# Performance work log

Hardware: AMD Instinct MI355X
Metric: run time of the kernel (lower is better)

## Reference

```python
import jax, jax.numpy as jnp
import numpy as np

B, S, D, H = 4, 2048, 1024, 16
HD = D // H  # head_dim = 64

def setup_inputs() -> dict:
    key = jax.random.key(0)
    ks = jax.random.split(key, 6)
    scale = 1.0 / np.sqrt(D)
    x = jax.random.normal(ks[0], (B, S, D), dtype=jnp.float32)
    Wq = jax.random.normal(ks[1], (D, D), dtype=jnp.float32) * scale
    Wk = jax.random.normal(ks[2], (D, D), dtype=jnp.float32) * scale
    Wv = jax.random.normal(ks[3], (D, D), dtype=jnp.float32) * scale
    Wo = jax.random.normal(ks[4], (D, D), dtype=jnp.float32) * scale
    z = jnp.zeros((D,), dtype=jnp.float32)
    return {"x": x, "Wq": Wq, "bq": z, "Wk": Wk, "bk": z, "Wv": Wv, "bv": z, "Wo": Wo, "bo": z}

def reference(x, Wq, bq, Wk, bk, Wv, bv, Wo, bo):
    b, s, d = x.shape
    hd = d // H
    def split_heads(t):
        return t.reshape(b, s, H, hd).swapaxes(1, 2)  # [B,H,S,hd]
    q = split_heads(x @ Wq + bq)
    k = split_heads(x @ Wk + bk)
    v = split_heads(x @ Wv + bv)
    logits = jnp.einsum('bhqd,bhkd->bhqk', q, k) / jnp.sqrt(jnp.asarray(hd, x.dtype))
    attn = jax.nn.softmax(logits, axis=-1)
    vals = jnp.einsum('bhqk,bhkd->bhqd', attn, v)
    vals = vals.swapaxes(1, 2).reshape(b, s, d)
    return vals @ Wo + bo
```

## Files before the change

### kernel.cpp

```cpp
#include <hip/hip_runtime.h>
#include <hip/hip_bf16.h>
#include <cstdint>
#include <cstddef>


typedef __attribute__((ext_vector_type(8))) short short8;
typedef __attribute__((ext_vector_type(8))) unsigned short ushort8;
typedef __attribute__((ext_vector_type(4))) unsigned short ushort4v;
typedef __attribute__((ext_vector_type(4))) float floatx4;

#define LOG2E 1.44269504088896340736f
#define QSCALE (0.125f * LOG2E)

__device__ __forceinline__ unsigned short f2bf(float f) {
  union { float f; unsigned int u; } c; c.f = f;
  return (unsigned short)((c.u + 0x7fffu + ((c.u >> 16) & 1u)) >> 16);
}

__device__ __forceinline__ unsigned int pack_bf16(float a, float b) {
  unsigned int ua = __builtin_bit_cast(unsigned int, a) + 0x8000u;
  unsigned int ub = __builtin_bit_cast(unsigned int, b) + 0x8000u;
  return __builtin_amdgcn_perm(ub, ua, 0x07060302);
}

__device__ __forceinline__ float fexp2(float x) {
#if __HIP_DEVICE_COMPILE__
  return __builtin_amdgcn_exp2f(x);
#else
  return x;
#endif
}

__device__ __forceinline__ void gl_lds16(const void* g, void* l) {
  __builtin_amdgcn_global_load_lds((__attribute__((address_space(1))) void*)g,
                                   (__attribute__((address_space(3))) void*)l, 16, 0, 0);
}

__global__ __launch_bounds__(256) void cast_x_kernel(const float* __restrict__ x,
                                                     unsigned short* __restrict__ xb, int n4) {
  int i = blockIdx.x * 256 + threadIdx.x;
  if (i >= n4) return;
  float4 v = ((const float4*)x)[i];
  ushort4v o;
  o.x = f2bf(v.x); o.y = f2bf(v.y); o.z = f2bf(v.z); o.w = f2bf(v.w);
  ((ushort4v*)xb)[i] = o;
}

__global__ __launch_bounds__(256) void transpose_w_kernel(
    const float* __restrict__ Wq, const float* __restrict__ Wk,
    const float* __restrict__ Wv, const float* __restrict__ Wo,
    unsigned short* __restrict__ Wqkv_t, unsigned short* __restrict__ Wo_t) {
  __shared__ float tile[32][33];
  const int which = blockIdx.z;
  const float* src = (which == 0) ? Wq : (which == 1) ? Wk : (which == 2) ? Wv : Wo;
  unsigned short* dst = (which == 3) ? Wo_t : (Wqkv_t + (size_t)which * 1024 * 1024);
  const int bn = blockIdx.x * 32;
  const int bk = blockIdx.y * 32;
  const int tx = threadIdx.x & 31, ty = threadIdx.x >> 5;
#pragma unroll
  for (int r = 0; r < 32; r += 8)
    tile[ty + r][tx] = src[(size_t)(bk + ty + r) * 1024 + bn + tx];
  __syncthreads();
#pragma unroll
  for (int r = 0; r < 32; r += 8)
    dst[(size_t)(bn + ty + r) * 1024 + bk + tx] = f2bf(tile[tx][ty + r]);
}

template <int MODE>
__global__ __launch_bounds__(256, 3) void gemm_bt(
    const unsigned short* __restrict__ A, const unsigned short* __restrict__ Bt,
    int M, int N, int K,
    const float* __restrict__ bias0, const float* __restrict__ bias1,
    const float* __restrict__ bias2,
    unsigned short* __restrict__ outQ, unsigned short* __restrict__ outK,
    unsigned short* __restrict__ outVt, float* __restrict__ outF) {
  __shared__ unsigned short As[128 * 32];
  __shared__ unsigned short Bs[128 * 32];

  const int tid = threadIdx.x;
  const int lane = tid & 63;
  const int wid = tid >> 6;
  const int wm = wid >> 1, wn = wid & 1;
  const int l15 = lane & 15, q4 = lane >> 4;
  const int bm = blockIdx.x * 128, bn = blockIdx.y * 128;

  const int rowL = lane >> 2;
  const int segL = (lane & 3) * 16;

  const char* Ab = (const char*)A;
  const char* Bb = (const char*)Bt;
  const size_t strideA = (size_t)K * 2;

  floatx4 acc[4][4] = {};

  for (int k0 = 0; k0 < K; k0 += 32) {
    __syncthreads();
#pragma unroll
    for (int c0 = 0; c0 < 2; ++c0) {
      const int c = wid * 2 + c0;
      gl_lds16(Ab + (size_t)(bm + c * 16 + rowL) * strideA + (size_t)k0 * 2 + segL,
               &As[c * 512]);
      gl_lds16(Bb + (size_t)(bn + c * 16 + rowL) * strideA + (size_t)k0 * 2 + segL,
               &Bs[c * 512]);
    }
    __syncthreads();

    short8 af[4], bfr[4];
#pragma unroll
    for (int i = 0; i < 4; ++i)
      af[i] = *(const short8*)&As[(wm * 64 + i * 16 + l15) * 32 + q4 * 8];
#pragma unroll
    for (int j = 0; j < 4; ++j)
      bfr[j] = *(const short8*)&Bs[(wn * 64 + j * 16 + l15) * 32 + q4 * 8];
#pragma unroll
    for (int i = 0; i < 4; ++i)
#pragma unroll
      for (int j = 0; j < 4; ++j)
        acc[i][j] = __builtin_amdgcn_mfma_f32_16x16x32_bf16(af[i], bfr[j], acc[i][j], 0, 0, 0);
  }

  if (MODE == 0) {
    __syncthreads();
    unsigned short* scr = ((wid < 2) ? As : Bs) + (wid & 1) * 2048;
    const int region = bn >> 10;
    const float* bias = (region == 0) ? bias0 : (region == 1) ? bias1 : bias2;
    const int row0b = bm + wm * 64;
    const int b = row0b >> 11;
    const int colbase = (bn + wn * 64) & 1023;
    const int h = colbase >> 6;
    const size_t bh = (size_t)(b * 16 + h);
#pragma unroll
    for (int i = 0; i < 4; ++i) {
      const int s0 = (row0b + i * 16) & 2047;
#pragma unroll
      for (int j = 0; j < 4; ++j) {
        const int col = j * 16 + l15;
        const float bb = bias[colbase + col];
#pragma unroll
        for (int r = 0; r < 4; ++r) {
          float v = acc[i][j][r] + bb;
          if (region == 0) v *= QSCALE;
          scr[(q4 * 4 + r) * 66 + col] = f2bf(v);
        }
      }
      if (region <= 1) {
        unsigned short* dst = (region == 0) ? outQ : outK;
        ushort8 v0 = *(ushort8*)&scr[l15 * 66 + q4 * 16];
        ushort8 v1 = *(ushort8*)&scr[l15 * 66 + q4 * 16 + 8];
        unsigned short* orow = dst + (bh * 2048 + s0 + l15) * 64 + q4 * 16;
        *(ushort8*)orow = v0;
        *(ushort8*)(orow + 8) = v1;
      } else {
        const int hd = lane;
        unsigned short tmp[16];
#pragma unroll
        for (int r = 0; r < 16; ++r) tmp[r] = scr[r * 66 + hd];
        ushort8 v0, v1;
#pragma unroll
        for (int r = 0; r < 8; ++r) { v0[r] = tmp[r]; v1[r] = tmp[8 + r]; }
        unsigned short* orow = outVt + (bh * 64 + hd) * 2048 + s0;
        *(ushort8*)orow = v0;
        *(ushort8*)(orow + 8) = v1;
      }
      __syncthreads();
    }
  } else {
#pragma unroll
    for (int i = 0; i < 4; ++i) {
      const int row0 = bm + wm * 64 + i * 16 + q4 * 4;
#pragma unroll
      for (int j = 0; j < 4; ++j) {
        const int gn = bn + wn * 64 + j * 16 + l15;
        const float bb = bias0[gn];
#pragma unroll
        for (int r = 0; r < 4; ++r)
          outF[(size_t)(row0 + r) * N + gn] = acc[i][j][r] + bb;
      }
    }
  }
}

__global__ __launch_bounds__(256, 4) void flash_attn(
    const unsigned short* __restrict__ Q, const unsigned short* __restrict__ Kg,
    const unsigned short* __restrict__ Vt, unsigned short* __restrict__ Oout) {
  __shared__ __align__(128) unsigned short Ks[2][64 * 64];
  __shared__ __align__(128) unsigned short Vs[2][64 * 64];

  const int tid = threadIdx.x, lane = tid & 63, wid = tid >> 6;
  const int l15 = lane & 15, q4 = lane >> 4;

  const int lid = blockIdx.x;
  const int slot = lid >> 3;
  const int bh = (lid & 7) * 8 + (slot >> 4);
  const int q0 = (slot & 15) * 128;
  const int bb = bh >> 4, hh = bh & 15;
  const size_t base = (size_t)bh * 2048 * 64;

  short8 qf[2][2];
#pragma unroll
  for (int s = 0; s < 2; ++s) {
    const unsigned short* qrow = Q + base + (size_t)(q0 + s * 64 + wid * 16 + l15) * 64;
    qf[s][0] = *(const short8*)(qrow + q4 * 8);
    qf[s][1] = *(const short8*)(qrow + 32 + q4 * 8);
  }

  union { unsigned int u[4]; short8 v; } ov;
  ov.u[0] = 0x3F803F80u; ov.u[1] = 0x3F803F80u; ov.u[2] = 0x3F803F80u; ov.u[3] = 0x3F803F80u;
  const short8 onesf = ov.v;

  const int r0 = wid * 16 + (lane >> 3);
  const int sg2 = ((lane & 7) ^ ((lane >> 3) & 7)) * 8;
  auto gpf = [](int r) {
    const int loc = r & 31;
    return (r & 32) + ((loc >> 2) & 3) * 8 + ((loc >> 4) & 1) * 4 + (loc & 3);
  };
  const unsigned short* kc0 = Kg + base + (size_t)gpf(r0) * 64 + sg2;
  const unsigned short* kc1 = Kg + base + (size_t)gpf(r0 + 8) * 64 + sg2;
  const unsigned short* vc0 = Vt + base + (size_t)r0 * 2048 + sg2;
  const unsigned short* vc1 = vc0 + 8 * 2048;

  const int wofs = wid * 1024;
  auto stage = [&](int b) {
    gl_lds16(kc0, &Ks[b][wofs]);        gl_lds16(kc1, &Ks[b][wofs + 512]);
    gl_lds16(vc0, &Vs[b][wofs]);        gl_lds16(vc1, &Vs[b][wofs + 512]);
    kc0 += 4096; kc1 += 4096; vc0 += 64; vc1 += 64;
  };

  stage(0);

  floatx4 oacc[2][4] = {};
  floatx4 lacc[2] = {};
  const int fo0 = (q4 ^ (l15 & 7)) << 3;

  const int thr = l15 * 64;
  const unsigned short* kA = &Ks[0][thr + fo0];
  const unsigned short* kB = &Ks[0][thr + (fo0 ^ 32)];
  const unsigned short* vA = &Vs[0][thr + fo0];
  const unsigned short* vB = &Vs[0][thr + (fo0 ^ 32)];

  auto body = [&](int BUF) {
    short8 pf[2][2];
#pragma unroll
    for (int c = 0; c < 2; ++c) {
      floatx4 sc[2][2] = {};
#pragma unroll
      for (int tt = 0; tt < 2; ++tt) {
        const int t = 2 * c + tt;
        short8 kf0 = *(const short8*)(kA + BUF + t * 1024);
        short8 kf1 = *(const short8*)(kB + BUF + t * 1024);
        __builtin_amdgcn_s_setprio(1);
#pragma unroll
        for (int s = 0; s < 2; ++s) {
          sc[s][tt] = __builtin_amdgcn_mfma_f32_16x16x32_bf16(kf0, qf[s][0], sc[s][tt], 0, 0, 0);
          sc[s][tt] = __builtin_amdgcn_mfma_f32_16x16x32_bf16(kf1, qf[s][1], sc[s][tt], 0, 0, 0);
        }
        __builtin_amdgcn_s_setprio(0);
      }
#pragma unroll
      for (int s = 0; s < 2; ++s) {
        float e0 = fexp2(sc[s][0][0]), e1 = fexp2(sc[s][0][1]);
        float e2 = fexp2(sc[s][0][2]), e3 = fexp2(sc[s][0][3]);
        float e4 = fexp2(sc[s][1][0]), e5 = fexp2(sc[s][1][1]);
        float e6 = fexp2(sc[s][1][2]), e7 = fexp2(sc[s][1][3]);
        union { unsigned int u[4]; short8 v; } cv;
        cv.u[0] = pack_bf16(e0, e1); cv.u[1] = pack_bf16(e2, e3);
        cv.u[2] = pack_bf16(e4, e5); cv.u[3] = pack_bf16(e6, e7);
        pf[s][c] = cv.v;
        lacc[s] = __builtin_amdgcn_mfma_f32_16x16x32_bf16(onesf, pf[s][c], lacc[s], 0, 0, 0);
      }
    }

#pragma unroll
    for (int t = 0; t < 4; ++t) {
      short8 vf0 = *(const short8*)(vA + BUF + t * 1024);
      short8 vf1 = *(const short8*)(vB + BUF + t * 1024);
      __builtin_amdgcn_s_setprio(1);
#pragma unroll
      for (int s = 0; s < 2; ++s) {
        oacc[s][t] = __builtin_amdgcn_mfma_f32_16x16x32_bf16(vf0, pf[s][0], oacc[s][t], 0, 0, 0);
        oacc[s][t] = __builtin_amdgcn_mfma_f32_16x16x32_bf16(vf1, pf[s][1], oacc[s][t], 0, 0, 0);
      }
      __builtin_amdgcn_s_setprio(0);
    }
  };

  for (int ip = 0; ip < 16; ++ip) {
    __syncthreads();
    stage(1);
    body(0);
    __syncthreads();
    if (ip < 15) stage(0);
    body(4096);
  }

#pragma unroll
  for (int s = 0; s < 2; ++s) {
    const float inv = 1.0f / lacc[s][0];
    const int srow = q0 + s * 64 + wid * 16 + l15;
    unsigned short* orow = Oout + ((size_t)bb * 2048 + srow) * 1024 + hh * 64;
#pragma unroll
    for (int t = 0; t < 4; ++t) {
      union { unsigned int u[2]; ushort4v s4; } cv;
      cv.u[0] = pack_bf16(oacc[s][t][0] * inv, oacc[s][t][1] * inv);
      cv.u[1] = pack_bf16(oacc[s][t][2] * inv, oacc[s][t][3] * inv);
      *(ushort4v*)(orow + t * 16 + q4 * 4) = cv.s4;
    }
  }
}

extern "C" void kernel_launch(void* const* d_in, const int* in_sizes, int n_in,
                              void* d_out, int out_size, void* d_ws, size_t ws_size,
                              hipStream_t stream) {
  const float* x  = (const float*)d_in[0];
  const float* Wq = (const float*)d_in[1];
  const float* bq = (const float*)d_in[2];
  const float* Wk = (const float*)d_in[3];
  const float* bk = (const float*)d_in[4];
  const float* Wv = (const float*)d_in[5];
  const float* bv = (const float*)d_in[6];
  const float* Wo = (const float*)d_in[7];
  const float* bo = (const float*)d_in[8];
  float* out = (float*)d_out;

  char* ws = (char*)d_ws;
  unsigned short* xb     = (unsigned short*)(ws);
  unsigned short* wqkv_t = (unsigned short*)(ws + (16u << 20));
  unsigned short* wo_t   = (unsigned short*)(ws + (22u << 20));
  unsigned short* Qb     = (unsigned short*)(ws + (24u << 20));
  unsigned short* Kb     = (unsigned short*)(ws + (40u << 20));
  unsigned short* Vtb    = (unsigned short*)(ws + (56u << 20));
  unsigned short* attn   = (unsigned short*)(ws + (72u << 20));
  (void)in_sizes; (void)n_in; (void)out_size; (void)ws_size;

  cast_x_kernel<<<dim3(8192), 256, 0, stream>>>(x, xb, 8192 * 1024 / 4);
  transpose_w_kernel<<<dim3(32, 32, 4), 256, 0, stream>>>(Wq, Wk, Wv, Wo, wqkv_t, wo_t);
  gemm_bt<0><<<dim3(64, 24), 256, 0, stream>>>(xb, wqkv_t, 8192, 3072, 1024,
                                               bq, bk, bv, Qb, Kb, Vtb, nullptr);
  flash_attn<<<dim3(1024), 256, 0, stream>>>(Qb, Kb, Vtb, attn);
  gemm_bt<1><<<dim3(64, 8), 256, 0, stream>>>(attn, wo_t, 8192, 1024, 1024,
                                              bo, nullptr, nullptr,
                                              nullptr, nullptr, nullptr, out);
}
```

Before: 271.0 us.

## Replace QKV projection GEMM with 256x256-tile 8-wave pipelined kernel

Adds a dedicated QKV GEMM kernel that uses 512 threads and 256x256 output tiles with a 64-wide K step. It double-buffers A and B through XOR-swizzled LDS via direct global-to-LDS loads, interleaving staging with MFMA bursts under raised wave priority. Larger tiles raise operand reuse and cut global traffic, and the swizzle avoids LDS bank conflicts. The cost is heavy register and LDS use (128 KB shared), which limits occupancy, and only 384 blocks are launched.

```diff
diff --git a/kernel.cpp b/kernel.cpp
--- a/kernel.cpp
+++ b/kernel.cpp
@@ -66,14 +66,146 @@
     dst[(size_t)(bn + ty + r) * 1024 + bk + tx] = f2bf(tile[tx][ty + r]);
 }
 
+#define QKV_FIRE(B0, B1, J0)                                                            \
+  __builtin_amdgcn_s_barrier();                                                         \
+  asm volatile("s_waitcnt lgkmcnt(0)" ::: "memory");                                    \
+  __builtin_amdgcn_sched_barrier(0);                                                    \
+  __builtin_amdgcn_s_setprio(1);                                                        \
+  _Pragma("unroll")                                                                     \
+  for (int i_ = 0; i_ < 8; ++i_) {                                                      \
+    acc[i_][J0] = __builtin_amdgcn_mfma_f32_16x16x32_bf16(af[i_], B0, acc[i_][J0], 0, 0, 0); \
+    acc[i_][J0 + 1] =                                                                   \
+        __builtin_amdgcn_mfma_f32_16x16x32_bf16(af[i_], B1, acc[i_][J0 + 1], 0, 0, 0);  \
+  }                                                                                     \
+  __builtin_amdgcn_s_setprio(0);
+
+__global__ __launch_bounds__(512, 2) void gemm_qkv8(
+    const unsigned short* __restrict__ A, const unsigned short* __restrict__ Bt,
+    const float* __restrict__ bq, const float* __restrict__ bk, const float* __restrict__ bv,
+    unsigned short* __restrict__ outQ, unsigned short* __restrict__ outK,
+    unsigned short* __restrict__ outVt) {
+  __shared__ __align__(128) unsigned short S[65536];
+
+  const int tid = threadIdx.x, lane = tid & 63, wid = tid >> 6;
+  const int wm = wid >> 2, wn = wid & 3;
+  const int l15 = lane & 15, q4 = lane >> 4;
+  const int bm = blockIdx.x * 256, bn = blockIdx.y * 256;
+
+  const int srow = wid * 16 + (lane >> 3);
+  const int sgu = ((lane & 7) ^ ((lane >> 3) & 7)) * 8;
+  const unsigned short* pa00 = A + (size_t)(bm + srow) * 1024 + sgu;
+  const unsigned short* pa01 = pa00 + 8 * 1024;
+  const unsigned short* pa10 = pa00 + 128 * 1024;
+  const unsigned short* pa11 = pa00 + 136 * 1024;
+  const unsigned short* pb00 = Bt + (size_t)(bn + srow) * 1024 + sgu;
+  const unsigned short* pb01 = pb00 + 8 * 1024;
+  const unsigned short* pb10 = pb00 + 128 * 1024;
+  const unsigned short* pb11 = pb00 + 136 * 1024;
+
+  const int wdst = wid * 1024;
+  auto stageA = [&](const int SO) {
+    gl_lds16(pa00, &S[SO + wdst]);          gl_lds16(pa01, &S[SO + wdst + 512]);
+    gl_lds16(pa10, &S[SO + 8192 + wdst]);   gl_lds16(pa11, &S[SO + 8192 + wdst + 512]);
+    pa00 += 64; pa01 += 64; pa10 += 64; pa11 += 64;
+  };
+  auto stageB = [&](const int SO) {
+    gl_lds16(pb00, &S[32768 + SO + wdst]);        gl_lds16(pb01, &S[32768 + SO + wdst + 512]);
+    gl_lds16(pb10, &S[32768 + SO + 8192 + wdst]); gl_lds16(pb11, &S[32768 + SO + 8192 + wdst + 512]);
+    pb00 += 64; pb01 += 64; pb10 += 64; pb11 += 64;
+  };
+
+  const int fo0 = (q4 ^ (l15 & 7)) * 8;
+  const unsigned short* aP0 = S + wm * 8192 + l15 * 64 + fo0;
+  const unsigned short* aP1 = S + wm * 8192 + l15 * 64 + (fo0 ^ 32);
+  const unsigned short* bP0 = S + 32768 + (wn >> 1) * 8192 + ((wn & 1) * 64 + l15) * 64 + fo0;
+  const unsigned short* bP1 = S + 32768 + (wn >> 1) * 8192 + ((wn & 1) * 64 + l15) * 64 + (fo0 ^ 32);
+
+  floatx4 acc[8][4] = {};
+  short8 af[8];
+
+  stageA(0); stageB(0);
+  __syncthreads();
+
+  auto body = [&](const int RO, const int SO) {
+#pragma unroll
+    for (int i = 0; i < 8; ++i) af[i] = *(const short8*)(aP0 + RO + i * 1024);
+    short8 b0 = *(const short8*)(bP0 + RO);
+    short8 b1 = *(const short8*)(bP0 + RO + 1024);
+    stageA(SO);
+    QKV_FIRE(b0, b1, 0)
+    __builtin_amdgcn_s_barrier();
+    b0 = *(const short8*)(bP0 + RO + 2048);
+    b1 = *(const short8*)(bP0 + RO + 3072);
+    stageB(SO);
+    QKV_FIRE(b0, b1, 2)
+    __builtin_amdgcn_s_barrier();
+#pragma unroll
+    for (int i = 0; i < 8; ++i) af[i] = *(const short8*)(aP1 + RO + i * 1024);
+    b0 = *(const short8*)(bP1 + RO);
+    b1 = *(const short8*)(bP1 + RO + 1024);
+    QKV_FIRE(b0, b1, 0)
+    __builtin_amdgcn_s_barrier();
+    b0 = *(const short8*)(bP1 + RO + 2048);
+    b1 = *(const short8*)(bP1 + RO + 3072);
+    QKV_FIRE(b0, b1, 2)
+    __syncthreads();
+  };
+
+  for (int p = 0; p < 8; ++p) {
+    body(0, 16384);
+    body(16384, 0);
+  }
+
+  __syncthreads();
+  unsigned short* scr = S + wid * 1088;
+  const int region = bn >> 10;
+  const float* bias = (region == 0) ? bq : (region == 1) ? bk : bv;
+  const int row0b = bm + wm * 128;
+  const int b = row0b >> 11;
+  const int colbase = (bn + wn * 64) & 1023;
+  const int h = colbase >> 6;
+  const size_t bh = (size_t)(b * 16 + h);
+#pragma unroll
+  for (int i = 0; i < 8; ++i) {
+    const int s0 = (row0b + i * 16) & 2047;
+#pragma unroll
+    for (int j = 0; j < 4; ++j) {
+      const int col = j * 16 + l15;
+      const float bb = bias[colbase + col];
+#pragma unroll
+      for (int r = 0; r < 4; ++r) {
+        float v = acc[i][j][r] + bb;
+        if (region == 0) v *= QSCALE;
+        scr[(q4 * 4 + r) * 66 + col] = f2bf(v);
+      }
+    }
+    if (region <= 1) {
+      unsigned short* dst = (region == 0) ? outQ : outK;
+      ushort8 v0 = *(ushort8*)&scr[l15 * 66 + q4 * 16];
+      ushort8 v1 = *(ushort8*)&scr[l15 * 66 + q4 * 16 + 8];
+      unsigned short* orow = dst + (bh * 2048 + s0 + l15) * 64 + q4 * 16;
+      *(ushort8*)orow = v0;
+      *(ushort8*)(orow + 8) = v1;
+    } else {
+      const int hd = lane;
+      unsigned short tmp[16];
+#pragma unroll
+      for (int r = 0; r < 16; ++r) tmp[r] = scr[r * 66 + hd];
+      ushort8 v0, v1;
+#pragma unroll
+      for (int r = 0; r < 8; ++r) { v0[r] = tmp[r]; v1[r] = tmp[8 + r]; }
+      unsigned short* orow = outVt + (bh * 64 + hd) * 2048 + s0;
+      *(ushort8*)orow = v0;
+      *(ushort8*)(orow + 8) = v1;
+    }
+  }
+}
+
 template <int MODE>
 __global__ __launch_bounds__(256, 3) void gemm_bt(
     const unsigned short* __restrict__ A, const unsigned short* __restrict__ Bt,
     int M, int N, int K,
-    const float* __restrict__ bias0, const float* __restrict__ bias1,
-    const float* __restrict__ bias2,
-    unsigned short* __restrict__ outQ, unsigned short* __restrict__ outK,
-    unsigned short* __restrict__ outVt, float* __restrict__ outF) {
+    const float* __restrict__ bias0, float* __restrict__ outF) {
   __shared__ unsigned short As[128 * 32];
   __shared__ unsigned short Bs[128 * 32];
 
@@ -119,63 +251,16 @@
         acc[i][j] = __builtin_amdgcn_mfma_f32_16x16x32_bf16(af[i], bfr[j], acc[i][j], 0, 0, 0);
   }
 
-  if (MODE == 0) {
-    __syncthreads();
-    unsigned short* scr = ((wid < 2) ? As : Bs) + (wid & 1) * 2048;
-    const int region = bn >> 10;
-    const float* bias = (region == 0) ? bias0 : (region == 1) ? bias1 : bias2;
-    const int row0b = bm + wm * 64;
-    const int b = row0b >> 11;
-    const int colbase = (bn + wn * 64) & 1023;
-    const int h = colbase >> 6;
-    const size_t bh = (size_t)(b * 16 + h);
-#pragma unroll
-    for (int i = 0; i < 4; ++i) {
-      const int s0 = (row0b + i * 16) & 2047;
-#pragma unroll
-      for (int j = 0; j < 4; ++j) {
-        const int col = j * 16 + l15;
-        const float bb = bias[colbase + col];
-#pragma unroll
-        for (int r = 0; r < 4; ++r) {
-          float v = acc[i][j][r] + bb;
-          if (region == 0) v *= QSCALE;
-          scr[(q4 * 4 + r) * 66 + col] = f2bf(v);
-        }
-      }
-      if (region <= 1) {
-        unsigned short* dst = (region == 0) ? outQ : outK;
-        ushort8 v0 = *(ushort8*)&scr[l15 * 66 + q4 * 16];
-        ushort8 v1 = *(ushort8*)&scr[l15 * 66 + q4 * 16 + 8];
-        unsigned short* orow = dst + (bh * 2048 + s0 + l15) * 64 + q4 * 16;
-        *(ushort8*)orow = v0;
-        *(ushort8*)(orow + 8) = v1;
-      } else {
-        const int hd = lane;
-        unsigned short tmp[16];
-#pragma unroll
-        for (int r = 0; r < 16; ++r) tmp[r] = scr[r * 66 + hd];
-        ushort8 v0, v1;
-#pragma unroll
-        for (int r = 0; r < 8; ++r) { v0[r] = tmp[r]; v1[r] = tmp[8 + r]; }
-        unsigned short* orow = outVt + (bh * 64 + hd) * 2048 + s0;
-        *(ushort8*)orow = v0;
-        *(ushort8*)(orow + 8) = v1;
-      }
-      __syncthreads();
-    }
-  } else {
-#pragma unroll
-    for (int i = 0; i < 4; ++i) {
-      const int row0 = bm + wm * 64 + i * 16 + q4 * 4;
-#pragma unroll
-      for (int j = 0; j < 4; ++j) {
-        const int gn = bn + wn * 64 + j * 16 + l15;
-        const float bb = bias0[gn];
-#pragma unroll
-        for (int r = 0; r < 4; ++r)
-          outF[(size_t)(row0 + r) * N + gn] = acc[i][j][r] + bb;
-      }
+#pragma unroll
+  for (int i = 0; i < 4; ++i) {
+    const int row0 = bm + wm * 64 + i * 16 + q4 * 4;
+#pragma unroll
+    for (int j = 0; j < 4; ++j) {
+      const int gn = bn + wn * 64 + j * 16 + l15;
+      const float bb = bias0[gn];
+#pragma unroll
+      for (int r = 0; r < 4; ++r)
+        outF[(size_t)(row0 + r) * N + gn] = acc[i][j][r] + bb;
     }
   }
 }
@@ -334,10 +419,7 @@
 
   cast_x_kernel<<<dim3(8192), 256, 0, stream>>>(x, xb, 8192 * 1024 / 4);
   transpose_w_kernel<<<dim3(32, 32, 4), 256, 0, stream>>>(Wq, Wk, Wv, Wo, wqkv_t, wo_t);
-  gemm_bt<0><<<dim3(64, 24), 256, 0, stream>>>(xb, wqkv_t, 8192, 3072, 1024,
-                                               bq, bk, bv, Qb, Kb, Vtb, nullptr);
+  gemm_qkv8<<<dim3(32, 12), 512, 0, stream>>>(xb, wqkv_t, bq, bk, bv, Qb, Kb, Vtb);
   flash_attn<<<dim3(1024), 256, 0, stream>>>(Qb, Kb, Vtb, attn);
-  gemm_bt<1><<<dim3(64, 8), 256, 0, stream>>>(attn, wo_t, 8192, 1024, 1024,
-                                              bo, nullptr, nullptr,
-                                              nullptr, nullptr, nullptr, out);
-}
+  gemm_bt<1><<<dim3(64, 8), 256, 0, stream>>>(attn, wo_t, 8192, 1024, 1024, bo, out);
+}
```

After: 276.8 us. +2.2%, slower.
